# Kernel tuning notes

Measured on AMD Instinct MI355X. Metric: run time of the kernel, lower is better.

The kernel has to match this reference:

```python
import jax, jax.numpy as jnp
import numpy as np

B, N, C, H, W = 256, 50000, 3, 32, 32


def setup_inputs() -> dict:
    key = jax.random.key(0)
    k1, k2, k3 = jax.random.split(key, 3)
    inp = jax.random.normal(k1, (B, C, H, W), dtype=jnp.float32)
    train_data = jax.random.normal(k2, (N, C, H, W), dtype=jnp.float32)
    # per-query noise levels in a realistic diffusion range
    sigma = jax.random.uniform(k3, (B,), dtype=jnp.float32) * 1.5 + 0.5
    return {"input": inp, "sigma": sigma, "train_data": train_data}


def reference(input, sigma, train_data):
    """Karras optimal denoiser:
    D(x, sigma) = sum_i y_i * Gau(x; y_i, sigma^2 I) / sum_i Gau(x; y_i, sigma^2 I).
    The Gaussian normalization constant (sigma*sqrt(2*pi))^D cancels in the ratio,
    so this is exactly softmax over -0.5*||x - y_i||^2 / sigma^2 (same math as the
    per-dim product of densities in the original, computed stably in log space).
    """
    b = input.shape[0]
    x = input.reshape(b, -1)                      # [B, D]
    y = train_data.reshape(train_data.shape[0], -1)  # [N, D]
    x2 = jnp.sum(x * x, axis=1, keepdims=True)    # [B, 1]
    y2 = jnp.sum(y * y, axis=1)                   # [N]
    # pairwise squared distances via GEMM: [B, N]
    sqdist = x2 + y2[None, :] - 2.0 * (x @ y.T)
    logw = -0.5 * sqdist / (sigma[:, None] ** 2)  # [B, N]
    w = jax.nn.softmax(logw, axis=1)              # normalized Gaussian weights
    out = w @ y                                   # [B, D] weighted average
    return out.reshape(input.shape)
```

## Files before the change

### kernel.cpp

```cpp
#include <hip/hip_runtime.h>
#include <hip/hip_bf16.h>
#include <type_traits>

#define BQ   256
#define NTR  50000
#define DD   3072
#define NSP  50048
#define NBLK 782
#define CAP  4096
#define DELTA 18.0f

typedef __fp16 f16;
typedef __fp16 f16x2 __attribute__((ext_vector_type(2)));
typedef __fp16 f16x4 __attribute__((ext_vector_type(4)));
typedef __fp16 f16x8 __attribute__((ext_vector_type(8)));
typedef float  f32x4 __attribute__((ext_vector_type(4)));

__global__ __launch_bounds__(256) void kx(const float* __restrict__ x, f16* __restrict__ xp) {
    const int t = blockIdx.x * 256 + threadIdx.x;
    const int g = t >> 8, r = t & 255;
    const f32x4* src = (const f32x4*)(x + (size_t)r * DD + (g << 3));
    f32x4 a = src[0], b = src[1];
    union { f16x2 h2[4]; f16x8 h8; } u;
    u.h2[0] = __builtin_amdgcn_cvt_pkrtz(a[0], a[1]);
    u.h2[1] = __builtin_amdgcn_cvt_pkrtz(a[2], a[3]);
    u.h2[2] = __builtin_amdgcn_cvt_pkrtz(b[0], b[1]);
    u.h2[3] = __builtin_amdgcn_cvt_pkrtz(b[2], b[3]);
    ((f16x8*)xp)[t] = u.h8;
}

__global__ __launch_bounds__(512, 4) void kqk(
    const f16* __restrict__ xp, const float* __restrict__ y,
    f16* __restrict__ S, float* __restrict__ pmax) {
    __shared__ char Bs[2][8192];

    const int tid = threadIdx.x;
    const int orig = blockIdx.x;
    const int xcd = orig & 7, cidx = orig >> 3;
    const int blk = (xcd < 6 ? xcd * 98 : 588 + (xcd - 6) * 97) + cidx;
    const int n0  = blk * 64;

    const int ry0 = tid >> 4;
    const int kc  = tid & 15;
    const int yr0 = n0 + ry0, yr1 = yr0 + 32;
    const bool yv0 = yr0 < NTR, yv1 = yr1 < NTR;
    const float* yb0 = y + (size_t)yr0 * DD + (kc << 2);
    const float* yb1 = y + (size_t)yr1 * DD + (kc << 2);
    const int swz = (ry0 & 7) << 4;
    const int bo0 = ry0 * 128        + (((((kc >> 1) << 4)) ^ swz) | ((kc & 1) << 3));
    const int bo1 = (ry0 + 32) * 128 + (((((kc >> 1) << 4)) ^ swz) | ((kc & 1) << 3));

    const int w = tid >> 6, l = tid & 63;
    const int l15 = l & 15, lg = l >> 4;

    f32x4 acc[2][4] = {};
    float y2a0 = 0.f, y2a1 = 0.f;
    f32x4 p0, p1, q0, q1;

    auto loady = [&](f32x4& a0, f32x4& a1, int ks) {
        a0 = yv0 ? *(const f32x4*)(yb0 + (ks << 6)) : f32x4(0.f);
        a1 = yv1 ? *(const f32x4*)(yb1 + (ks << 6)) : f32x4(0.f);
    };
    auto cvtw = [&](f32x4& a0, f32x4& a1, int buf) {
        y2a0 += a0[0]*a0[0] + a0[1]*a0[1] + a0[2]*a0[2] + a0[3]*a0[3];
        y2a1 += a1[0]*a1[0] + a1[1]*a1[1] + a1[2]*a1[2] + a1[3]*a1[3];
        union { f16x2 h2[2]; f16x4 h4; } u0, u1;
        u0.h2[0] = __builtin_amdgcn_cvt_pkrtz(a0[0], a0[1]);
        u0.h2[1] = __builtin_amdgcn_cvt_pkrtz(a0[2], a0[3]);
        u1.h2[0] = __builtin_amdgcn_cvt_pkrtz(a1[0], a1[1]);
        u1.h2[1] = __builtin_amdgcn_cvt_pkrtz(a1[2], a1[3]);
        *(f16x4*)(&Bs[buf][bo0]) = u0.h4;
        *(f16x4*)(&Bs[buf][bo1]) = u1.h4;
    };

    loady(p0, p1, 0);
    loady(q0, q1, 1);
    cvtw(p0, p1, 0);
    asm volatile("s_waitcnt lgkmcnt(0)" ::: "memory");
    __builtin_amdgcn_s_barrier();

    const f16x8* ap = (const f16x8*)xp;
    const int arow = (w << 5) + l15;

    auto iter = [&](int ks, auto curC,
                    f32x4& s0, f32x4& s1,
                    f32x4& t0, f32x4& t1) {
        constexpr int cur = decltype(curC)::value;
        f16x8 af[2][2];
        #pragma unroll
        for (int kk = 0; kk < 2; ++kk)
            #pragma unroll
            for (int fm = 0; fm < 2; ++fm)
                af[kk][fm] = ap[(size_t)((ks << 3) + (kk << 2) + lg) * 256 + arow + (fm << 4)];
        if (ks + 2 < 48) loady(s0, s1, ks + 2);
        f16x8 bf[2][4];
        #pragma unroll
        for (int kk = 0; kk < 2; ++kk)
            #pragma unroll
            for (int fn = 0; fn < 4; ++fn) {
                int r = (fn << 4) + l15;
                bf[kk][fn] = *(const f16x8*)(&Bs[cur][r * 128 + (((kk << 6) + (lg << 4)) ^ ((r & 7) << 4))]);
            }
        #pragma unroll
        for (int kk = 0; kk < 2; ++kk)
            #pragma unroll
            for (int fm = 0; fm < 2; ++fm)
                #pragma unroll
                for (int fn = 0; fn < 4; ++fn)
                    acc[fm][fn] = __builtin_amdgcn_mfma_f32_16x16x32_f16(af[kk][fm], bf[kk][fn], acc[fm][fn], 0, 0, 0);
        if (ks + 1 < 48) cvtw(t0, t1, cur ^ 1);
        asm volatile("s_waitcnt lgkmcnt(0)" ::: "memory");
        __builtin_amdgcn_s_barrier();
    };

    for (int ks2 = 0; ks2 < 48; ks2 += 2) {
        iter(ks2,     std::integral_constant<int,0>{}, p0, p1, q0, q1);
        iter(ks2 + 1, std::integral_constant<int,1>{}, q0, q1, p0, p1);
    }

    float* lys = (float*)&Bs[0][0];
    #pragma unroll
    for (int off = 1; off < 16; off <<= 1) {
        y2a0 += __shfl_xor(y2a0, off, 64);
        y2a1 += __shfl_xor(y2a1, off, 64);
    }
    if ((tid & 15) == 0) { lys[ry0] = y2a0; lys[ry0 + 32] = y2a1; }
    __syncthreads();
    float ly2[4];
    #pragma unroll
    for (int fn = 0; fn < 4; ++fn) ly2[fn] = 0.5f * lys[(fn << 4) + l15];
    #pragma unroll
    for (int fm = 0; fm < 2; ++fm) {
        #pragma unroll
        for (int j = 0; j < 4; ++j) {
            float rm = -3.4e38f;
            #pragma unroll
            for (int fn = 0; fn < 4; ++fn) {
                int col = n0 + (fn << 4) + l15;
                float sc = acc[fm][fn][j] - ly2[fn];
                rm = (col < NTR) ? fmaxf(rm, sc) : rm;
            }
            #pragma unroll
            for (int off = 1; off < 16; off <<= 1) rm = fmaxf(rm, __shfl_xor(rm, off, 64));
            if (l15 == 0)
                pmax[(size_t)((w << 5) + (fm << 4) + (lg << 2) + j) * NBLK + blk] = rm;
        }
    }
    #pragma unroll
    for (int fm = 0; fm < 2; ++fm) {
        int row0 = (w << 5) + (fm << 4) + (lg << 2);
        #pragma unroll
        for (int fn = 0; fn < 4; ++fn) {
            int col = n0 + (fn << 4) + l15;
            f16* sp = S + (size_t)row0 * NSP + col;
            sp[0]               = (f16)(acc[fm][fn][0] - ly2[fn]);
            sp[NSP]             = (f16)(acc[fm][fn][1] - ly2[fn]);
            sp[2 * (size_t)NSP] = (f16)(acc[fm][fn][2] - ly2[fn]);
            sp[3 * (size_t)NSP] = (f16)(acc[fm][fn][3] - ly2[fn]);
        }
    }
}

__global__ __launch_bounds__(512) void ksp(
    const float* __restrict__ x, const float* __restrict__ y,
    const f16* __restrict__ S, const float* __restrict__ pmax,
    const float* __restrict__ sig, float* __restrict__ out) {
    __shared__ float xs[DD];
    __shared__ unsigned ci[CAP];
    __shared__ unsigned scnt;
    __shared__ float red[8];
    __shared__ float om[8], ol[8];
    __shared__ float sumv[DD];
    const int b = blockIdx.x, tid = threadIdx.x;
    const float s2 = sig[b] * sig[b];
    const float isc = -0.5f / s2;
    const int w = tid >> 6, l = tid & 63;

    if (tid == 0) scnt = 0;
    for (int i = tid; i < DD; i += 512) xs[i] = x[(size_t)b * DD + i];
    const float* pm = pmax + (size_t)b * NBLK;
    float mx = -3.4e38f;
    for (int i = tid; i < NBLK; i += 512) mx = fmaxf(mx, pm[i]);
    #pragma unroll
    for (int o = 1; o < 64; o <<= 1) mx = fmaxf(mx, __shfl_xor(mx, o, 64));
    if (l == 0) red[w] = mx;
    __syncthreads();
    mx = red[0];
    #pragma unroll
    for (int ww = 1; ww < 8; ++ww) mx = fmaxf(mx, red[ww]);
    const float thr = mx - DELTA * s2 - 2.0f;

    const f16x8* row = (const f16x8*)(S + (size_t)b * NSP);
    for (int i = tid; i < 6256; i += 512) {
        f16x8 v = row[i];
        #pragma unroll
        for (int j = 0; j < 8; ++j) {
            int idx = (i << 3) + j;
            if ((float)v[j] >= thr && idx < NTR) {
                unsigned p = atomicAdd(&scnt, 1u);
                if (p < CAP) ci[p] = (unsigned)idx;
            }
        }
    }
    __syncthreads();
    const int c = (int)(scnt < (unsigned)CAP ? scnt : (unsigned)CAP);

    const f32x4* xr = (const f32x4*)xs;
    f32x4 o[12] = {};
    float m = -3.4e38f, ll = 0.f;
    f32x4 A[12], Bv[12];

    auto LD = [&](f32x4* dst, int i) {
        const f32x4* yr = (const f32x4*)(y + (size_t)ci[i] * DD);
        #pragma unroll
        for (int j = 0; j < 12; ++j) dst[j] = yr[(j << 6) + l];
    };
    auto PROC = [&](f32x4* src) {
        float d2 = 0.f;
        #pragma unroll
        for (int j = 0; j < 12; ++j) {
            f32x4 xv = xr[(j << 6) + l];
            float a0 = xv[0]-src[j][0], a1 = xv[1]-src[j][1],
                  a2 = xv[2]-src[j][2], a3 = xv[3]-src[j][3];
            d2 += a0*a0 + a1*a1 + a2*a2 + a3*a3;
        }
        #pragma unroll
        for (int off = 1; off < 64; off <<= 1) d2 += __shfl_xor(d2, off, 64);
        float s = d2 * isc;
        float mn = fmaxf(m, s);
        float f = __expf(m - mn);
        float wi = __expf(s - mn);
        #pragma unroll
        for (int j = 0; j < 12; ++j) o[j] = o[j] * f + wi * src[j];
        ll = ll * f + wi;
        m = mn;
    };

    int i = w;
    if (i < c) LD(A, i);
    for (; i < c; i += 16) {
        int i2 = i + 8;
        if (i2 < c) LD(Bv, i2);
        PROC(A);
        if (i2 < c) {
            if (i + 16 < c) LD(A, i + 16);
            PROC(Bv);
        }
    }
    om[w] = m; ol[w] = ll;
    __syncthreads();
    float M = om[0];
    #pragma unroll
    for (int ww = 1; ww < 8; ++ww) M = fmaxf(M, om[ww]);
    float Ls = 0.f;
    #pragma unroll
    for (int ww = 0; ww < 8; ++ww) Ls += ol[ww] * __expf(om[ww] - M);
    const float fw = __expf(m - M);
    f32x4* sv = (f32x4*)sumv;
    if (w == 0) {
        #pragma unroll
        for (int j = 0; j < 12; ++j) sv[(j << 6) + l] = o[j] * fw;
    }
    __syncthreads();
    for (int ww = 1; ww < 8; ++ww) {
        if (w == ww) {
            #pragma unroll
            for (int j = 0; j < 12; ++j) sv[(j << 6) + l] += o[j] * fw;
        }
        __syncthreads();
    }
    const float inv = 1.f / Ls;
    f32x4* od = (f32x4*)(out + (size_t)b * DD);
    for (int t = tid; t < 768; t += 512) od[t] = sv[t] * inv;
}

extern "C" void kernel_launch(void* const* d_in, const int* in_sizes, int n_in,
                              void* d_out, int out_size, void* d_ws, size_t ws_size,
                              hipStream_t stream) {
    const float* x   = (const float*)d_in[0];
    const float* sig = (const float*)d_in[1];
    const float* y   = (const float*)d_in[2];
    float* out = (float*)d_out;
    char* ws = (char*)d_ws;
    f16*   xp   = (f16*)(ws);
    float* pmax = (float*)(ws + 1572864);
    f16*   S    = (f16*)(ws + 2373632);

    kx  <<<384, 256, 0, stream>>>(x, xp);
    kqk <<<NBLK, 512, 0, stream>>>(xp, y, S, pmax);
    ksp <<<256, 512, 0, stream>>>(x, y, S, pmax, sig, out);
}
```

Baseline: 243.7 us.

## Warp-specialize QK kernel with producer waves feeding an 8-slot LDS ring

Splits the distance GEMM kernel into 8 consumer waves that run MFMAs and 4 producer waves that load fp32 training rows, convert them to fp16 into an 8-deep shared-memory ring, and accumulate squared norms. Per-slot LDS flags with spin-waits replace the block-wide barrier every k-step. The aim is to overlap global loads of y with matrix work and to avoid stalls when every wave waits on a barrier. In exchange the block grows to 768 threads, uses more LDS and fewer blocks per CU, and adds polling overhead plus the risk of subtle memory-ordering issues.

```diff
diff --git a/kernel.cpp b/kernel.cpp
--- a/kernel.cpp
+++ b/kernel.cpp
@@ -29,134 +29,161 @@
     ((f16x8*)xp)[t] = u.h8;
 }
 
-__global__ __launch_bounds__(512, 4) void kqk(
+__global__ __launch_bounds__(768, 3) void kqk(
     const f16* __restrict__ xp, const float* __restrict__ y,
     f16* __restrict__ S, float* __restrict__ pmax) {
-    __shared__ char Bs[2][8192];
+    __shared__ __align__(16) char ring[8][8192];
+    __shared__ int pflag[8][4];
+    __shared__ int cflag[8][8];
+    __shared__ float lysf[64];
 
     const int tid = threadIdx.x;
     const int orig = blockIdx.x;
     const int xcd = orig & 7, cidx = orig >> 3;
     const int blk = (xcd < 6 ? xcd * 98 : 588 + (xcd - 6) * 97) + cidx;
     const int n0  = blk * 64;
-
-    const int ry0 = tid >> 4;
-    const int kc  = tid & 15;
-    const int yr0 = n0 + ry0, yr1 = yr0 + 32;
-    const bool yv0 = yr0 < NTR, yv1 = yr1 < NTR;
-    const float* yb0 = y + (size_t)yr0 * DD + (kc << 2);
-    const float* yb1 = y + (size_t)yr1 * DD + (kc << 2);
-    const int swz = (ry0 & 7) << 4;
-    const int bo0 = ry0 * 128        + (((((kc >> 1) << 4)) ^ swz) | ((kc & 1) << 3));
-    const int bo1 = (ry0 + 32) * 128 + (((((kc >> 1) << 4)) ^ swz) | ((kc & 1) << 3));
-
     const int w = tid >> 6, l = tid & 63;
     const int l15 = l & 15, lg = l >> 4;
 
+    if (tid < 32) (&pflag[0][0])[tid] = 0;
+    else if (tid < 96) (&cflag[0][0])[tid - 32] = 0;
+    __syncthreads();
+
     f32x4 acc[2][4] = {};
-    float y2a0 = 0.f, y2a1 = 0.f;
-    f32x4 p0, p1, q0, q1;
-
-    auto loady = [&](f32x4& a0, f32x4& a1, int ks) {
-        a0 = yv0 ? *(const f32x4*)(yb0 + (ks << 6)) : f32x4(0.f);
-        a1 = yv1 ? *(const f32x4*)(yb1 + (ks << 6)) : f32x4(0.f);
-    };
-    auto cvtw = [&](f32x4& a0, f32x4& a1, int buf) {
-        y2a0 += a0[0]*a0[0] + a0[1]*a0[1] + a0[2]*a0[2] + a0[3]*a0[3];
-        y2a1 += a1[0]*a1[0] + a1[1]*a1[1] + a1[2]*a1[2] + a1[3]*a1[3];
-        union { f16x2 h2[2]; f16x4 h4; } u0, u1;
-        u0.h2[0] = __builtin_amdgcn_cvt_pkrtz(a0[0], a0[1]);
-        u0.h2[1] = __builtin_amdgcn_cvt_pkrtz(a0[2], a0[3]);
-        u1.h2[0] = __builtin_amdgcn_cvt_pkrtz(a1[0], a1[1]);
-        u1.h2[1] = __builtin_amdgcn_cvt_pkrtz(a1[2], a1[3]);
-        *(f16x4*)(&Bs[buf][bo0]) = u0.h4;
-        *(f16x4*)(&Bs[buf][bo1]) = u1.h4;
-    };
-
-    loady(p0, p1, 0);
-    loady(q0, q1, 1);
-    cvtw(p0, p1, 0);
-    asm volatile("s_waitcnt lgkmcnt(0)" ::: "memory");
-    __builtin_amdgcn_s_barrier();
-
-    const f16x8* ap = (const f16x8*)xp;
-    const int arow = (w << 5) + l15;
-
-    auto iter = [&](int ks, auto curC,
-                    f32x4& s0, f32x4& s1,
-                    f32x4& t0, f32x4& t1) {
-        constexpr int cur = decltype(curC)::value;
-        f16x8 af[2][2];
-        #pragma unroll
-        for (int kk = 0; kk < 2; ++kk)
-            #pragma unroll
-            for (int fm = 0; fm < 2; ++fm)
-                af[kk][fm] = ap[(size_t)((ks << 3) + (kk << 2) + lg) * 256 + arow + (fm << 4)];
-        if (ks + 2 < 48) loady(s0, s1, ks + 2);
-        f16x8 bf[2][4];
-        #pragma unroll
-        for (int kk = 0; kk < 2; ++kk)
-            #pragma unroll
-            for (int fn = 0; fn < 4; ++fn) {
-                int r = (fn << 4) + l15;
-                bf[kk][fn] = *(const f16x8*)(&Bs[cur][r * 128 + (((kk << 6) + (lg << 4)) ^ ((r & 7) << 4))]);
-            }
-        #pragma unroll
-        for (int kk = 0; kk < 2; ++kk)
-            #pragma unroll
-            for (int fm = 0; fm < 2; ++fm)
-                #pragma unroll
-                for (int fn = 0; fn < 4; ++fn)
-                    acc[fm][fn] = __builtin_amdgcn_mfma_f32_16x16x32_f16(af[kk][fm], bf[kk][fn], acc[fm][fn], 0, 0, 0);
-        if (ks + 1 < 48) cvtw(t0, t1, cur ^ 1);
-        asm volatile("s_waitcnt lgkmcnt(0)" ::: "memory");
-        __builtin_amdgcn_s_barrier();
-    };
-
-    for (int ks2 = 0; ks2 < 48; ks2 += 2) {
-        iter(ks2,     std::integral_constant<int,0>{}, p0, p1, q0, q1);
-        iter(ks2 + 1, std::integral_constant<int,1>{}, q0, q1, p0, p1);
-    }
-
-    float* lys = (float*)&Bs[0][0];
-    #pragma unroll
-    for (int off = 1; off < 16; off <<= 1) {
-        y2a0 += __shfl_xor(y2a0, off, 64);
-        y2a1 += __shfl_xor(y2a1, off, 64);
-    }
-    if ((tid & 15) == 0) { lys[ry0] = y2a0; lys[ry0 + 32] = y2a1; }
-    __syncthreads();
-    float ly2[4];
-    #pragma unroll
-    for (int fn = 0; fn < 4; ++fn) ly2[fn] = 0.5f * lys[(fn << 4) + l15];
-    #pragma unroll
-    for (int fm = 0; fm < 2; ++fm) {
-        #pragma unroll
-        for (int j = 0; j < 4; ++j) {
-            float rm = -3.4e38f;
+    float y2p[4] = {0.f, 0.f, 0.f, 0.f};
+    int rowid[4];
+
+    if (w < 8) {
+        const f16x8* ap = (const f16x8*)xp;
+        const int arow = (w << 5) + l15;
+        for (int ks = 0; ks < 48; ++ks) {
+            const int slot = ks & 7, e1 = (ks >> 3) + 1;
+            f16x8 af[2][2];
+            #pragma unroll
+            for (int kk = 0; kk < 2; ++kk)
+                #pragma unroll
+                for (int fm = 0; fm < 2; ++fm)
+                    af[kk][fm] = ap[(size_t)((ks << 3) + (kk << 2) + lg) * 256 + arow + (fm << 4)];
+            {
+                volatile int* pf = &pflag[slot][0];
+                while (!(pf[0] >= e1 && pf[1] >= e1 && pf[2] >= e1 && pf[3] >= e1))
+                    __builtin_amdgcn_s_sleep(2);
+            }
+            asm volatile("" ::: "memory");
+            const char* Bc = ring[slot];
+            f16x8 bf[2][4];
+            #pragma unroll
+            for (int kk = 0; kk < 2; ++kk)
+                #pragma unroll
+                for (int fn = 0; fn < 4; ++fn) {
+                    int r = (fn << 4) + l15;
+                    bf[kk][fn] = *(const f16x8*)(&Bc[r * 128 + (((kk << 6) + (lg << 4)) ^ ((r & 7) << 4))]);
+                }
+            #pragma unroll
+            for (int kk = 0; kk < 2; ++kk)
+                #pragma unroll
+                for (int fm = 0; fm < 2; ++fm)
+                    #pragma unroll
+                    for (int fn = 0; fn < 4; ++fn)
+                        acc[fm][fn] = __builtin_amdgcn_mfma_f32_16x16x32_f16(af[kk][fm], bf[kk][fn], acc[fm][fn], 0, 0, 0);
+            asm volatile("s_waitcnt lgkmcnt(0)" ::: "memory");
+            if (l == 0) *(volatile int*)&cflag[slot][w] = e1;
+        }
+    } else {
+        const int pw = w - 8;
+        const int r4 = l >> 4;
+        const int kc = l & 15;
+        const float* yb[4];
+        #pragma unroll
+        for (int p = 0; p < 4; ++p) {
+            int row = (pw << 4) + (p << 2) + r4;
+            rowid[p] = row;
+            int gr = n0 + row; gr = gr < NTR ? gr : NTR - 1;
+            yb[p] = y + (size_t)gr * DD + (kc << 2);
+        }
+        f32x4 P[4], Q[4];
+        auto pload = [&](f32x4 (&D)[4], int ks) {
+            #pragma unroll
+            for (int p = 0; p < 4; ++p) D[p] = *(const f32x4*)(yb[p] + (ks << 6));
+        };
+        auto PITER = [&](int ks, f32x4 (&CUR)[4]) {
+            const int slot = ks & 7, e = ks >> 3;
+            if (e > 0) {
+                volatile int* cf = &cflag[slot][0];
+                while (!(cf[0] >= e && cf[1] >= e && cf[2] >= e && cf[3] >= e &&
+                         cf[4] >= e && cf[5] >= e && cf[6] >= e && cf[7] >= e))
+                    __builtin_amdgcn_s_sleep(1);
+            }
+            asm volatile("" ::: "memory");
+            if (ks < 47) asm volatile("s_waitcnt vmcnt(4)" ::: "memory");
+            else         asm volatile("s_waitcnt vmcnt(0)" ::: "memory");
+            #pragma unroll
+            for (int p = 0; p < 4; ++p) {
+                f32x4 v = CUR[p];
+                y2p[p] += v[0]*v[0] + v[1]*v[1] + v[2]*v[2] + v[3]*v[3];
+                union { f16x2 h2[2]; f16x4 h4; } u;
+                u.h2[0] = __builtin_amdgcn_cvt_pkrtz(v[0], v[1]);
+                u.h2[1] = __builtin_amdgcn_cvt_pkrtz(v[2], v[3]);
+                int row = rowid[p];
+                int bo = row * 128 + ((((kc >> 1) << 4) ^ ((row & 7) << 4)) | ((kc & 1) << 3));
+                *(f16x4*)(&ring[slot][bo]) = u.h4;
+            }
+            asm volatile("s_waitcnt lgkmcnt(0)" ::: "memory");
+            if (l == 0) *(volatile int*)&pflag[slot][pw] = e + 1;
+            if (ks + 2 < 48) pload(CUR, ks + 2);
+        };
+        pload(P, 0); pload(Q, 1);
+        for (int ks2 = 0; ks2 < 48; ks2 += 2) { PITER(ks2, P); PITER(ks2 + 1, Q); }
+        #pragma unroll
+        for (int p = 0; p < 4; ++p) {
+            float v = y2p[p];
+            v += __shfl_xor(v, 1, 64);
+            v += __shfl_xor(v, 2, 64);
+            v += __shfl_xor(v, 4, 64);
+            v += __shfl_xor(v, 8, 64);
+            y2p[p] = v;
+        }
+    }
+    __syncthreads();
+    if (w >= 8 && (l & 15) == 0) {
+        #pragma unroll
+        for (int p = 0; p < 4; ++p) lysf[rowid[p]] = y2p[p];
+    }
+    __syncthreads();
+
+    if (w < 8) {
+        float ly2[4];
+        #pragma unroll
+        for (int fn = 0; fn < 4; ++fn) ly2[fn] = 0.5f * lysf[(fn << 4) + l15];
+        #pragma unroll
+        for (int fm = 0; fm < 2; ++fm) {
+            #pragma unroll
+            for (int j = 0; j < 4; ++j) {
+                float rm = -3.4e38f;
+                #pragma unroll
+                for (int fn = 0; fn < 4; ++fn) {
+                    int col = n0 + (fn << 4) + l15;
+                    float sc = acc[fm][fn][j] - ly2[fn];
+                    rm = (col < NTR) ? fmaxf(rm, sc) : rm;
+                }
+                #pragma unroll
+                for (int off = 1; off < 16; off <<= 1) rm = fmaxf(rm, __shfl_xor(rm, off, 64));
+                if (l15 == 0)
+                    pmax[(size_t)((w << 5) + (fm << 4) + (lg << 2) + j) * NBLK + blk] = rm;
+            }
+        }
+        #pragma unroll
+        for (int fm = 0; fm < 2; ++fm) {
+            int row0 = (w << 5) + (fm << 4) + (lg << 2);
             #pragma unroll
             for (int fn = 0; fn < 4; ++fn) {
                 int col = n0 + (fn << 4) + l15;
-                float sc = acc[fm][fn][j] - ly2[fn];
-                rm = (col < NTR) ? fmaxf(rm, sc) : rm;
-            }
-            #pragma unroll
-            for (int off = 1; off < 16; off <<= 1) rm = fmaxf(rm, __shfl_xor(rm, off, 64));
-            if (l15 == 0)
-                pmax[(size_t)((w << 5) + (fm << 4) + (lg << 2) + j) * NBLK + blk] = rm;
-        }
-    }
-    #pragma unroll
-    for (int fm = 0; fm < 2; ++fm) {
-        int row0 = (w << 5) + (fm << 4) + (lg << 2);
-        #pragma unroll
-        for (int fn = 0; fn < 4; ++fn) {
-            int col = n0 + (fn << 4) + l15;
-            f16* sp = S + (size_t)row0 * NSP + col;
-            sp[0]               = (f16)(acc[fm][fn][0] - ly2[fn]);
-            sp[NSP]             = (f16)(acc[fm][fn][1] - ly2[fn]);
-            sp[2 * (size_t)NSP] = (f16)(acc[fm][fn][2] - ly2[fn]);
-            sp[3 * (size_t)NSP] = (f16)(acc[fm][fn][3] - ly2[fn]);
+                f16* sp = S + (size_t)row0 * NSP + col;
+                sp[0]               = (f16)(acc[fm][fn][0] - ly2[fn]);
+                sp[NSP]             = (f16)(acc[fm][fn][1] - ly2[fn]);
+                sp[2 * (size_t)NSP] = (f16)(acc[fm][fn][2] - ly2[fn]);
+                sp[3 * (size_t)NSP] = (f16)(acc[fm][fn][3] - ly2[fn]);
+            }
         }
     }
 }
@@ -287,6 +314,6 @@
     f16*   S    = (f16*)(ws + 2373632);
 
     kx  <<<384, 256, 0, stream>>>(x, xp);
-    kqk <<<NBLK, 512, 0, stream>>>(xp, y, S, pmax);
+    kqk <<<NBLK, 768, 0, stream>>>(xp, y, S, pmax);
     ksp <<<256, 512, 0, stream>>>(x, y, S, pmax, sig, out);
 }
```

After: 321.2 us. +31.8%, slower.
